# Optimization experiments

Measured on AMD Instinct MI355X. Metric: run time of the kernel, lower is better.

The kernel has to match this reference:

```python
import jax, jax.numpy as jnp
import numpy as np
from jax import lax

EPS = 1e-5


def _conv(x, w, b, stride, pad):
    # x: [B,C,H,W], w: [O,I,kh,kw] (NCHW / OIHW, same as torch Conv2d)
    y = lax.conv_general_dilated(
        x, w, window_strides=stride,
        padding=[(pad[0], pad[0]), (pad[1], pad[1])],
        dimension_numbers=('NCHW', 'OIHW', 'NCHW'))
    return y + b[None, :, None, None]


def _bn(x, gamma, beta, mean, var):
    # BatchNorm2d in eval mode (running statistics)
    inv = gamma / jnp.sqrt(var + EPS)
    return x * inv[None, :, None, None] + (beta - mean * inv)[None, :, None, None]


def _mask_time(x, lens):
    # Vectorized replacement of the per-sample narrow/fill loop:
    # zero every time step >= lens[b] along the last axis.
    t = jnp.arange(x.shape[3])
    keep = (t[None, :] < lens[:, None]).astype(x.dtype)  # [B, W]
    return x * keep[:, None, None, :]


def _new_len(lens, kernel_w, stride_w, pad_w):
    # matches get_new_sequence_lengths for Conv2d with dilation 1
    return (lens + 2 * pad_w - (kernel_w - 1) - 1) // stride_w + 1


def _forward(inputs, seq_lengths,
             w1, b1, g1, be1, m1, v1,
             w2, b2, g2, be2, m2, v2):
    lens = seq_lengths.astype(jnp.int32)
    # layer 1: Conv2d(1,32,(41,11),(2,2),(20,5))
    x = _conv(inputs, w1, b1, (2, 2), (20, 5))
    lens = _new_len(lens, 11, 2, 5)
    x = _mask_time(x, lens)
    # BatchNorm2d(32) -> mask
    x = _mask_time(_bn(x, g1, be1, m1, v1), lens)
    # Hardtanh(0,20) -> mask
    x = _mask_time(jnp.clip(x, 0.0, 20.0), lens)
    # layer 2: Conv2d(32,32,(21,11),(2,1),(10,5))
    x = _conv(x, w2, b2, (2, 1), (10, 5))
    lens = _new_len(lens, 11, 1, 5)
    x = _mask_time(x, lens)
    x = _mask_time(_bn(x, g2, be2, m2, v2), lens)
    x = _mask_time(jnp.clip(x, 0.0, 20.0), lens)
    return x, lens


def setup_inputs() -> dict:
    key = jax.random.key(0)
    ks = jax.random.split(key, 8)
    inputs = jax.random.normal(ks[0], (32, 1, 161, 1024), dtype=jnp.float32)
    seq_lengths = jax.random.randint(ks[1], (32,), 1, 1024, dtype=jnp.int32)
    w1 = jax.random.normal(ks[2], (32, 1, 41, 11), dtype=jnp.float32) * 0.05
    b1 = jax.random.normal(ks[3], (32,), dtype=jnp.float32) * 0.05
    w2 = jax.random.normal(ks[4], (32, 32, 21, 11), dtype=jnp.float32) * 0.02
    b2 = jax.random.normal(ks[5], (32,), dtype=jnp.float32) * 0.05
    g1 = jnp.ones((32,), jnp.float32)
    be1 = jnp.zeros((32,), jnp.float32)
    m1 = jax.random.normal(ks[6], (32,), dtype=jnp.float32) * 0.1
    v1 = jnp.ones((32,), jnp.float32)
    g2 = jnp.ones((32,), jnp.float32)
    be2 = jnp.zeros((32,), jnp.float32)
    m2 = jax.random.normal(ks[7], (32,), dtype=jnp.float32) * 0.1
    v2 = jnp.ones((32,), jnp.float32)
    return {"inputs": inputs, "seq_lengths": seq_lengths,
            "w1": w1, "b1": b1, "g1": g1, "be1": be1, "m1": m1, "v1": v1,
            "w2": w2, "b2": b2, "g2": g2, "be2": be2, "m2": m2, "v2": v2}


def reference(inputs, seq_lengths, w1, b1, g1, be1, m1, v1,
              w2, b2, g2, be2, m2, v2):
    return _forward(inputs, seq_lengths, w1, b1, g1, be1, m1, v1,
                    w2, b2, g2, be2, m2, v2)
```

## Files before the change

### kernel.cpp

```cpp
#include <hip/hip_runtime.h>
#include <math.h>

#define B_    32
#define H_IN  161
#define W_IN  1024
#define C1_   32
#define H1_   81
#define W1_   512
#define C2_   32
#define H2_   41
#define W2_   512

#define OUT_X_SZ ((size_t)B_ * C2_ * H2_ * W2_)

#define WF2_B    0u
#define WF1_B    563200u
#define SCSH_B   609280u
#define LENS1_B  609792u
#define XG_B     609920u

#define WF2_N    281600
#define WF1_N    23040

typedef __bf16 v8bf __attribute__((ext_vector_type(8)));
typedef float v16f __attribute__((ext_vector_type(16)));

static __device__ __forceinline__ unsigned short f2bf(float f) {
    unsigned int u = __float_as_uint(f);
    unsigned int r = (u + 0x7fffu + ((u >> 16) & 1u)) >> 16;
    return (unsigned short)r;
}

__global__ void prep_kernel(const float* __restrict__ w1, const float* __restrict__ b1,
                            const float* __restrict__ g1, const float* __restrict__ be1,
                            const float* __restrict__ m1, const float* __restrict__ v1,
                            const float* __restrict__ w2, const float* __restrict__ b2,
                            const float* __restrict__ g2, const float* __restrict__ be2,
                            const float* __restrict__ m2, const float* __restrict__ v2,
                            const int* __restrict__ lens,
                            unsigned short* __restrict__ wf1, unsigned short* __restrict__ wf2,
                            float* __restrict__ scsh, int* __restrict__ lens1,
                            float* __restrict__ out_lens)
{
    const int i = blockIdx.x * blockDim.x + threadIdx.x;
    const int stride = gridDim.x * blockDim.x;

    for (int idx = i; idx < WF2_N; idx += stride) {
        int j  = idx & 7;
        int l  = (idx >> 3) & 63;
        int f  = idx >> 9;
        int ch = f & 1;
        int kwkh = f >> 1;
        int kw  = kwkh % 11;
        int khp = kwkh / 11;
        int kh  = khp - 2;
        int oc = l & 31;
        int c  = ch * 16 + ((l >> 5) << 3) + j;
        wf2[idx] = (kh >= 0 && kh < 21)
                 ? f2bf(w2[((oc * 32 + c) * 21 + kh) * 11 + kw]) : (unsigned short)0;
    }
    for (int idx = i; idx < WF1_N; idx += stride) {
        int j   = idx & 7;
        int l   = (idx >> 3) & 63;
        int khp = idx >> 9;
        int kh  = khp - 2;
        int k   = ((l >> 5) << 3) + j;
        int oc  = l & 31;
        wf1[idx] = (k < 11 && kh >= 0 && kh < 41)
                 ? f2bf(w1[oc * 451 + kh * 11 + k]) : (unsigned short)0;
    }
    if (i < 32) {
        float s1 = g1[i] / sqrtf(v1[i] + 1e-5f);
        scsh[i]      = s1;
        scsh[32 + i] = b1[i] * s1 + be1[i] - m1[i] * s1;
        float s2 = g2[i] / sqrtf(v2[i] + 1e-5f);
        scsh[64 + i] = s2;
        scsh[96 + i] = b2[i] * s2 + be2[i] - m2[i] * s2;
        int l1 = (lens[i] - 1) / 2 + 1;
        if (l1 > W1_) l1 = W1_;
        lens1[i] = l1;
        out_lens[i] = (float)l1;
    }
}

__global__ __launch_bounds__(256) void conv1_mfma(
    const float* __restrict__ x,
    const unsigned short* __restrict__ wf1,
    const float* __restrict__ scsh,
    const int* __restrict__ lens1,
    unsigned short* __restrict__ xg)
{
    const int t    = threadIdx.x;
    const int lane = t & 63;
    const int l31  = lane & 31;
    const int lhi  = lane >> 5;
    const int wv   = t >> 6;
    const int w0   = blockIdx.x * 256;
    const int hp   = blockIdx.y;
    const int b    = blockIdx.z;
    const int h0   = hp * 2;
    const bool h1ok = (h0 + 1) < H1_;

    __shared__ unsigned int srow[2][264];

    v16f acc[2][2];
#pragma unroll
    for (int hh = 0; hh < 2; ++hh)
#pragma unroll
        for (int nt = 0; nt < 2; ++nt)
#pragma unroll
            for (int q = 0; q < 16; ++q) acc[hh][nt][q] = 0.f;

    const int r0 = 2 * h0 - 20;
    const int cb = 2 * w0 - 5;
    const float* xb = x + (size_t)b * (H_IN * W_IN);

    const int dwbase = wv * 64 + l31 + 4 * lhi;

    {
        float a0 = 0.f, a1 = 0.f, c0v = 0.f, c1v = 0.f;
        if (r0 >= 0 && r0 < H_IN) {
            const float* src = xb + (size_t)r0 * W_IN;
            int c0 = cb + 2 * t;
            if ((unsigned)c0 < (unsigned)W_IN)       a0 = src[c0];
            if ((unsigned)(c0 + 1) < (unsigned)W_IN) a1 = src[c0 + 1];
            if (t < 7) {
                int c1 = cb + 2 * (256 + t);
                if ((unsigned)c1 < (unsigned)W_IN)       c0v = src[c1];
                if ((unsigned)(c1 + 1) < (unsigned)W_IN) c1v = src[c1 + 1];
            }
        }
        srow[0][t] = (unsigned int)f2bf(a0) | ((unsigned int)f2bf(a1) << 16);
        if (t < 7)
            srow[0][256 + t] = (unsigned int)f2bf(c0v) | ((unsigned int)f2bf(c1v) << 16);
    }
    __syncthreads();

    const uint4* wf1q = (const uint4*)wf1;

    for (int kp = 0; kp < 43; ++kp) {
        const int p = kp & 1;
        const int rn = r0 + kp + 1;
        const bool rv = (kp < 42) && (rn >= 0) && (rn < H_IN);

        float a0 = 0.f, a1 = 0.f, c0v = 0.f, c1v = 0.f;
        if (rv) {
            const float* src = xb + (size_t)rn * W_IN;
            int c0 = cb + 2 * t;
            if ((unsigned)c0 < (unsigned)W_IN)       a0 = src[c0];
            if ((unsigned)(c0 + 1) < (unsigned)W_IN) a1 = src[c0 + 1];
            if (t < 7) {
                int c1 = cb + 2 * (256 + t);
                if ((unsigned)c1 < (unsigned)W_IN)       c0v = src[c1];
                if ((unsigned)(c1 + 1) < (unsigned)W_IN) c1v = src[c1 + 1];
            }
        }

        const int r = r0 + kp;
        if (r >= 0 && r < H_IN) {
            uint4 a0u = wf1q[(kp + 2) * 32 + lane];
            uint4 a1u = wf1q[kp * 32 + lane];
            v8bf A0 = __builtin_bit_cast(v8bf, a0u);
            v8bf A1 = __builtin_bit_cast(v8bf, a1u);
            const unsigned int* bp = &srow[p][0];
            uint4 bu0, bu1;
            {
                int dw = dwbase;
                bu0.x = bp[dw]; bu0.y = bp[dw + 1]; bu0.z = bp[dw + 2]; bu0.w = bp[dw + 3];
                dw += 32;
                bu1.x = bp[dw]; bu1.y = bp[dw + 1]; bu1.z = bp[dw + 2]; bu1.w = bp[dw + 3];
            }
            v8bf B0 = __builtin_bit_cast(v8bf, bu0);
            v8bf B1 = __builtin_bit_cast(v8bf, bu1);
            acc[0][0] = __builtin_amdgcn_mfma_f32_32x32x16_bf16(A0, B0, acc[0][0], 0, 0, 0);
            acc[0][1] = __builtin_amdgcn_mfma_f32_32x32x16_bf16(A0, B1, acc[0][1], 0, 0, 0);
            acc[1][0] = __builtin_amdgcn_mfma_f32_32x32x16_bf16(A1, B0, acc[1][0], 0, 0, 0);
            acc[1][1] = __builtin_amdgcn_mfma_f32_32x32x16_bf16(A1, B1, acc[1][1], 0, 0, 0);
        }

        if (rv) {
            srow[p ^ 1][t] = (unsigned int)f2bf(a0) | ((unsigned int)f2bf(a1) << 16);
            if (t < 7)
                srow[p ^ 1][256 + t] = (unsigned int)f2bf(c0v) | ((unsigned int)f2bf(c1v) << 16);
        }
        __syncthreads();
    }

    const int l1 = lens1[b];
#pragma unroll
    for (int hh = 0; hh < 2; ++hh) {
        if (hh == 1 && !h1ok) break;
        const int h = h0 + hh;
#pragma unroll
        for (int nt = 0; nt < 2; ++nt) {
            const int w = w0 + wv * 64 + nt * 32 + l31;
            const bool keep = (w < l1);
            unsigned short* dp = xg + (((size_t)b * H1_ + h) * W1_ + w) * 32;
#pragma unroll
            for (int rq = 0; rq < 4; ++rq) {
                unsigned int wd[2];
#pragma unroll
                for (int d = 0; d < 2; ++d) {
                    int rg = rq * 4 + d * 2;
                    int oc = 8 * rq + 4 * lhi + d * 2;
                    float av0 = acc[hh][nt][rg];
                    float av1 = acc[hh][nt][rg + 1];
                    float v0 = fminf(fmaxf(fmaf(av0, scsh[oc],     scsh[32 + oc]), 0.f), 20.f);
                    float v1 = fminf(fmaxf(fmaf(av1, scsh[oc + 1], scsh[33 + oc]), 0.f), 20.f);
                    if (!keep) { v0 = 0.f; v1 = 0.f; }
                    wd[d] = (unsigned int)f2bf(v0) | ((unsigned int)f2bf(v1) << 16);
                }
                uint2 u; u.x = wd[0]; u.y = wd[1];
                *(uint2*)(dp + 8 * rq + 4 * lhi) = u;
            }
        }
    }
}

#define ROWB 21280

__global__ __launch_bounds__(256, 3) void conv2_mfma(
    const unsigned short* __restrict__ xg,
    const unsigned short* __restrict__ wf2,
    const float* __restrict__ scsh,
    const int* __restrict__ lens1,
    float* __restrict__ out)
{
    const int t    = threadIdx.x;
    const int lane = t & 63;
    const int l31  = lane & 31;
    const int lhi  = lane >> 5;
    const int wv   = t >> 6;

    const int id   = blockIdx.x;
    const int sid  = (id & 7) * 168 + (id >> 3);
    const int wblk = sid & 1;
    const int bh   = sid >> 1;
    const int hp   = bh % 21;
    const int b    = bh / 21;
    const int h0   = hp * 2;
    const bool h1ok = (h0 + 1) < H2_;
    const int w0B  = wblk << 8;

    __shared__ __align__(16) char sbuf[2 * ROWB];

    v16f acc[2][2];
#pragma unroll
    for (int hh = 0; hh < 2; ++hh)
#pragma unroll
        for (int nt = 0; nt < 2; ++nt)
#pragma unroll
            for (int q = 0; q < 16; ++q) acc[hh][nt][q] = 0.f;

    const int st_lds = (t >> 2) * 80 + (t & 3) * 16;
    const int rd_lds = (wv * 64 + l31) * 80 + lhi * 16;

    const unsigned short* xb = xg + (size_t)b * (H1_ * W1_ * 32);
    const int r0 = 2 * h0 - 10;

    {
        int r = r0;
        if (r >= 0 && r < H1_) {
            const unsigned short* xrow = xb + (size_t)r * (W1_ * 32);
#pragma unroll
            for (int it = 0; it < 5; ++it) {
                int i = t + it * 256;
                int wp = (i >> 2) + w0B - 5;
                uint4 z; z.x = z.y = z.z = z.w = 0u;
                if (i < 1064 && wp >= 0 && wp < W1_)
                    z = *(const uint4*)(xrow + (size_t)wp * 32 + (i & 3) * 8);
                if (i < 1064)
                    *(uint4*)(sbuf + st_lds + it * 5120) = z;
            }
        }
    }
    __syncthreads();

    const uint4* wq = (const uint4*)wf2;

    for (int kp = 0; kp < 23; ++kp) {
        const int p = kp & 1;
        const int rn = r0 + kp + 1;
        const bool stage_next = (kp < 22) && (rn >= 0) && (rn < H1_);

        uint4 g0, g1, g2, g3, g4;
        g0.x=g0.y=g0.z=g0.w=0u; g1=g0; g2=g0; g3=g0; g4=g0;
        if (stage_next) {
            const unsigned short* xrow = xb + (size_t)rn * (W1_ * 32);
            const int wbase = (t >> 2) + w0B - 5;
            const int ck = (t & 3) * 8;
            if (wbase >= 0 && wbase < W1_)                 g0 = *(const uint4*)(xrow + (size_t)wbase * 32 + ck);
            if (wbase + 64 >= 0 && wbase + 64 < W1_)       g1 = *(const uint4*)(xrow + (size_t)(wbase + 64) * 32 + ck);
            if (wbase + 128 < W1_)                         g2 = *(const uint4*)(xrow + (size_t)(wbase + 128) * 32 + ck);
            if (wbase + 192 < W1_)                         g3 = *(const uint4*)(xrow + (size_t)(wbase + 192) * 32 + ck);
            if (t < 40 && wbase + 256 < W1_)               g4 = *(const uint4*)(xrow + (size_t)(wbase + 256) * 32 + ck);
        }

        const int r = r0 + kp;
        if (r >= 0 && r < H1_) {
            const int f0 = (kp + 2) * 22;
            const int f1 = kp * 22;
            const char* bbase = sbuf + p * ROWB + rd_lds;
            __builtin_amdgcn_s_setprio(1);
#pragma unroll
            for (int kw = 0; kw < 11; ++kw) {
#pragma unroll
                for (int ch = 0; ch < 2; ++ch) {
                    uint4 a0u = wq[(f0 + kw * 2 + ch) * 64 + lane];
                    uint4 a1u = wq[(f1 + kw * 2 + ch) * 64 + lane];
                    uint4 b0u = *(const uint4*)(bbase + kw * 80 + ch * 32);
                    uint4 b1u = *(const uint4*)(bbase + 2560 + kw * 80 + ch * 32);
                    v8bf A0 = __builtin_bit_cast(v8bf, a0u);
                    v8bf A1 = __builtin_bit_cast(v8bf, a1u);
                    v8bf B0 = __builtin_bit_cast(v8bf, b0u);
                    v8bf B1 = __builtin_bit_cast(v8bf, b1u);
                    acc[0][0] = __builtin_amdgcn_mfma_f32_32x32x16_bf16(A0, B0, acc[0][0], 0, 0, 0);
                    acc[0][1] = __builtin_amdgcn_mfma_f32_32x32x16_bf16(A0, B1, acc[0][1], 0, 0, 0);
                    acc[1][0] = __builtin_amdgcn_mfma_f32_32x32x16_bf16(A1, B0, acc[1][0], 0, 0, 0);
                    acc[1][1] = __builtin_amdgcn_mfma_f32_32x32x16_bf16(A1, B1, acc[1][1], 0, 0, 0);
                }
            }
            __builtin_amdgcn_s_setprio(0);
        }

        if (stage_next) {
            char* wb = sbuf + (p ^ 1) * ROWB + st_lds;
            *(uint4*)(wb)            = g0;
            *(uint4*)(wb + 5120)     = g1;
            *(uint4*)(wb + 2 * 5120) = g2;
            *(uint4*)(wb + 3 * 5120) = g3;
            if (t < 40) *(uint4*)(wb + 4 * 5120) = g4;
        }
        __syncthreads();
    }

    const int l2 = lens1[b];
#pragma unroll
    for (int hh = 0; hh < 2; ++hh) {
        if (hh == 1 && !h1ok) break;
        const int h = h0 + hh;
#pragma unroll
        for (int nt = 0; nt < 2; ++nt) {
            const int w = w0B + wv * 64 + nt * 32 + l31;
            const bool keep = (w < l2);
#pragma unroll
            for (int reg = 0; reg < 16; ++reg) {
                const int oc = (reg & 3) + 8 * (reg >> 2) + 4 * lhi;
                float v = fmaf(acc[hh][nt][reg], scsh[64 + oc], scsh[96 + oc]);
                v = fminf(fmaxf(v, 0.f), 20.f);
                out[(((size_t)b * C2_ + oc) * H2_ + h) * W2_ + w] = keep ? v : 0.f;
            }
        }
    }
}

extern "C" void kernel_launch(void* const* d_in, const int* in_sizes, int n_in,
                              void* d_out, int out_size, void* d_ws, size_t ws_size,
                              hipStream_t stream) {
    const float* inputs = (const float*)d_in[0];
    const int*   slen   = (const int*)d_in[1];
    const float* w1 = (const float*)d_in[2];
    const float* b1 = (const float*)d_in[3];
    const float* g1 = (const float*)d_in[4];
    const float* be1 = (const float*)d_in[5];
    const float* m1 = (const float*)d_in[6];
    const float* v1 = (const float*)d_in[7];
    const float* w2 = (const float*)d_in[8];
    const float* b2 = (const float*)d_in[9];
    const float* g2 = (const float*)d_in[10];
    const float* be2 = (const float*)d_in[11];
    const float* m2 = (const float*)d_in[12];
    const float* v2 = (const float*)d_in[13];

    char* ws = (char*)d_ws;
    unsigned short* wf2  = (unsigned short*)(ws + WF2_B);
    unsigned short* wf1  = (unsigned short*)(ws + WF1_B);
    float*          scsh = (float*)(ws + SCSH_B);
    int*            lens1 = (int*)(ws + LENS1_B);
    unsigned short* xg   = (unsigned short*)(ws + XG_B);

    float* out_x    = (float*)d_out;
    float* out_lens = out_x + OUT_X_SZ;

    hipLaunchKernelGGL(prep_kernel, dim3(256), dim3(256), 0, stream,
                       w1, b1, g1, be1, m1, v1, w2, b2, g2, be2, m2, v2,
                       slen, wf1, wf2, scsh, lens1, out_lens);

    hipLaunchKernelGGL(conv1_mfma, dim3(2, 41, B_), dim3(256), 0, stream,
                       inputs, wf1, scsh, lens1, xg);

    hipLaunchKernelGGL(conv2_mfma, dim3(1344), dim3(256), 0, stream,
                       xg, wf2, scsh, lens1, out_x);
}
```

Measured before the change: 533.9 us.

## Stage a 55-row input slab in LDS and compute four output row pairs per block

conv1 now loads a slab of 55 input rows into shared memory once per block and computes four output row-pairs from it. Before, each block streamed 43 rows with a double-buffered row and a barrier per row. This cuts redundant global reads of overlapping input rows (about 4x reuse) and removes the per-row synchronisation. In exchange it uses about 58 KB of LDS per block, which limits occupancy (launch bounds ask for 2 blocks), and cuts the grid from 41 to 11 row segments, leaving fewer blocks to hide latency.

```diff
diff --git a/kernel.cpp b/kernel.cpp
--- a/kernel.cpp
+++ b/kernel.cpp
@@ -83,7 +83,10 @@
     }
 }
 
-__global__ __launch_bounds__(256) void conv1_mfma(
+#define S1ROWS 55
+#define S1U    264
+
+__global__ __launch_bounds__(256, 2) void conv1_mfma(
     const float* __restrict__ x,
     const unsigned short* __restrict__ wf1,
     const float* __restrict__ scsh,
@@ -96,73 +99,68 @@
     const int lhi  = lane >> 5;
     const int wv   = t >> 6;
     const int w0   = blockIdx.x * 256;
-    const int hp   = blockIdx.y;
+    const int seg  = blockIdx.y;
     const int b    = blockIdx.z;
-    const int h0   = hp * 2;
-    const bool h1ok = (h0 + 1) < H1_;
-
-    __shared__ unsigned int srow[2][264];
-
-    v16f acc[2][2];
-#pragma unroll
-    for (int hh = 0; hh < 2; ++hh)
-#pragma unroll
-        for (int nt = 0; nt < 2; ++nt)
-#pragma unroll
-            for (int q = 0; q < 16; ++q) acc[hh][nt][q] = 0.f;
-
-    const int r0 = 2 * h0 - 20;
-    const int cb = 2 * w0 - 5;
+
+    __shared__ unsigned int slab[S1ROWS * S1U];
+
+    const int rbase = 16 * seg - 20;
+    const int cb    = 2 * w0 - 5;
     const float* xb = x + (size_t)b * (H_IN * W_IN);
 
-    const int dwbase = wv * 64 + l31 + 4 * lhi;
-
-    {
-        float a0 = 0.f, a1 = 0.f, c0v = 0.f, c1v = 0.f;
-        if (r0 >= 0 && r0 < H_IN) {
-            const float* src = xb + (size_t)r0 * W_IN;
-            int c0 = cb + 2 * t;
-            if ((unsigned)c0 < (unsigned)W_IN)       a0 = src[c0];
-            if ((unsigned)(c0 + 1) < (unsigned)W_IN) a1 = src[c0 + 1];
-            if (t < 7) {
-                int c1 = cb + 2 * (256 + t);
-                if ((unsigned)c1 < (unsigned)W_IN)       c0v = src[c1];
-                if ((unsigned)(c1 + 1) < (unsigned)W_IN) c1v = src[c1 + 1];
-            }
-        }
-        srow[0][t] = (unsigned int)f2bf(a0) | ((unsigned int)f2bf(a1) << 16);
-        if (t < 7)
-            srow[0][256 + t] = (unsigned int)f2bf(c0v) | ((unsigned int)f2bf(c1v) << 16);
+    for (int rho = wv; rho < S1ROWS; rho += 4) {
+        const int r = rbase + rho;
+        const bool rowok = (r >= 0) && (r < H_IN);
+        const float* src = xb + (size_t)r * W_IN;
+        unsigned int* drow = &slab[rho * S1U];
+#pragma unroll
+        for (int j = 0; j < 4; ++j) {
+            const int cp = lane + 64 * j;
+            const int c  = cb + 2 * cp;
+            float a0 = 0.f, a1 = 0.f;
+            if (rowok) {
+                if ((unsigned)c < (unsigned)W_IN)       a0 = src[c];
+                if ((unsigned)(c + 1) < (unsigned)W_IN) a1 = src[c + 1];
+            }
+            drow[cp] = (unsigned int)f2bf(a0) | ((unsigned int)f2bf(a1) << 16);
+        }
+        if (lane < 8) {
+            const int cp = lane + 256;
+            const int c  = cb + 2 * cp;
+            float a0 = 0.f, a1 = 0.f;
+            if (rowok) {
+                if ((unsigned)c < (unsigned)W_IN)       a0 = src[c];
+                if ((unsigned)(c + 1) < (unsigned)W_IN) a1 = src[c + 1];
+            }
+            drow[cp] = (unsigned int)f2bf(a0) | ((unsigned int)f2bf(a1) << 16);
+        }
     }
     __syncthreads();
 
     const uint4* wf1q = (const uint4*)wf1;
-
-    for (int kp = 0; kp < 43; ++kp) {
-        const int p = kp & 1;
-        const int rn = r0 + kp + 1;
-        const bool rv = (kp < 42) && (rn >= 0) && (rn < H_IN);
-
-        float a0 = 0.f, a1 = 0.f, c0v = 0.f, c1v = 0.f;
-        if (rv) {
-            const float* src = xb + (size_t)rn * W_IN;
-            int c0 = cb + 2 * t;
-            if ((unsigned)c0 < (unsigned)W_IN)       a0 = src[c0];
-            if ((unsigned)(c0 + 1) < (unsigned)W_IN) a1 = src[c0 + 1];
-            if (t < 7) {
-                int c1 = cb + 2 * (256 + t);
-                if ((unsigned)c1 < (unsigned)W_IN)       c0v = src[c1];
-                if ((unsigned)(c1 + 1) < (unsigned)W_IN) c1v = src[c1 + 1];
-            }
-        }
-
-        const int r = r0 + kp;
-        if (r >= 0 && r < H_IN) {
+    const int dwbase  = wv * 64 + l31 + 4 * lhi;
+    const int l1      = lens1[b];
+
+    for (int q = 0; q < 4; ++q) {
+        const int pr = seg * 4 + q;
+        if (pr > 40) break;
+        const int h0 = pr * 2;
+        const bool h1ok = (h0 + 1) < H1_;
+
+        v16f acc[2][2];
+#pragma unroll
+        for (int hh = 0; hh < 2; ++hh)
+#pragma unroll
+            for (int nt = 0; nt < 2; ++nt)
+#pragma unroll
+                for (int qq = 0; qq < 16; ++qq) acc[hh][nt][qq] = 0.f;
+
+        const unsigned int* base = &slab[(4 * q) * S1U];
+
+        for (int kp = 0; kp < 43; ++kp) {
             uint4 a0u = wf1q[(kp + 2) * 32 + lane];
             uint4 a1u = wf1q[kp * 32 + lane];
-            v8bf A0 = __builtin_bit_cast(v8bf, a0u);
-            v8bf A1 = __builtin_bit_cast(v8bf, a1u);
-            const unsigned int* bp = &srow[p][0];
+            const unsigned int* bp = base + kp * S1U;
             uint4 bu0, bu1;
             {
                 int dw = dwbase;
@@ -170,6 +168,8 @@
                 dw += 32;
                 bu1.x = bp[dw]; bu1.y = bp[dw + 1]; bu1.z = bp[dw + 2]; bu1.w = bp[dw + 3];
             }
+            v8bf A0 = __builtin_bit_cast(v8bf, a0u);
+            v8bf A1 = __builtin_bit_cast(v8bf, a1u);
             v8bf B0 = __builtin_bit_cast(v8bf, bu0);
             v8bf B1 = __builtin_bit_cast(v8bf, bu1);
             acc[0][0] = __builtin_amdgcn_mfma_f32_32x32x16_bf16(A0, B0, acc[0][0], 0, 0, 0);
@@ -178,40 +178,32 @@
             acc[1][1] = __builtin_amdgcn_mfma_f32_32x32x16_bf16(A1, B1, acc[1][1], 0, 0, 0);
         }
 
-        if (rv) {
-            srow[p ^ 1][t] = (unsigned int)f2bf(a0) | ((unsigned int)f2bf(a1) << 16);
-            if (t < 7)
-                srow[p ^ 1][256 + t] = (unsigned int)f2bf(c0v) | ((unsigned int)f2bf(c1v) << 16);
-        }
-        __syncthreads();
-    }
-
-    const int l1 = lens1[b];
-#pragma unroll
-    for (int hh = 0; hh < 2; ++hh) {
-        if (hh == 1 && !h1ok) break;
-        const int h = h0 + hh;
-#pragma unroll
-        for (int nt = 0; nt < 2; ++nt) {
-            const int w = w0 + wv * 64 + nt * 32 + l31;
-            const bool keep = (w < l1);
-            unsigned short* dp = xg + (((size_t)b * H1_ + h) * W1_ + w) * 32;
-#pragma unroll
-            for (int rq = 0; rq < 4; ++rq) {
-                unsigned int wd[2];
-#pragma unroll
-                for (int d = 0; d < 2; ++d) {
-                    int rg = rq * 4 + d * 2;
-                    int oc = 8 * rq + 4 * lhi + d * 2;
-                    float av0 = acc[hh][nt][rg];
-                    float av1 = acc[hh][nt][rg + 1];
-                    float v0 = fminf(fmaxf(fmaf(av0, scsh[oc],     scsh[32 + oc]), 0.f), 20.f);
-                    float v1 = fminf(fmaxf(fmaf(av1, scsh[oc + 1], scsh[33 + oc]), 0.f), 20.f);
-                    if (!keep) { v0 = 0.f; v1 = 0.f; }
-                    wd[d] = (unsigned int)f2bf(v0) | ((unsigned int)f2bf(v1) << 16);
+#pragma unroll
+        for (int hh = 0; hh < 2; ++hh) {
+            if (hh == 1 && !h1ok) break;
+            const int h = h0 + hh;
+#pragma unroll
+            for (int nt = 0; nt < 2; ++nt) {
+                const int w = w0 + wv * 64 + nt * 32 + l31;
+                const bool keep = (w < l1);
+                unsigned short* dp = xg + (((size_t)b * H1_ + h) * W1_ + w) * 32;
+#pragma unroll
+                for (int rq = 0; rq < 4; ++rq) {
+                    unsigned int wd[2];
+#pragma unroll
+                    for (int d = 0; d < 2; ++d) {
+                        int rg = rq * 4 + d * 2;
+                        int oc = 8 * rq + 4 * lhi + d * 2;
+                        float av0 = acc[hh][nt][rg];
+                        float av1 = acc[hh][nt][rg + 1];
+                        float v0 = fminf(fmaxf(fmaf(av0, scsh[oc],     scsh[32 + oc]), 0.f), 20.f);
+                        float v1 = fminf(fmaxf(fmaf(av1, scsh[oc + 1], scsh[33 + oc]), 0.f), 20.f);
+                        if (!keep) { v0 = 0.f; v1 = 0.f; }
+                        wd[d] = (unsigned int)f2bf(v0) | ((unsigned int)f2bf(v1) << 16);
+                    }
+                    uint2 u; u.x = wd[0]; u.y = wd[1];
+                    *(uint2*)(dp + 8 * rq + 4 * lhi) = u;
                 }
-                uint2 u; u.x = wd[0]; u.y = wd[1];
-                *(uint2*)(dp + 8 * rq + 4 * lhi) = u;
             }
         }
     }
@@ -386,7 +378,7 @@
                        w1, b1, g1, be1, m1, v1, w2, b2, g2, be2, m2, v2,
                        slen, wf1, wf2, scsh, lens1, out_lens);
 
-    hipLaunchKernelGGL(conv1_mfma, dim3(2, 41, B_), dim3(256), 0, stream,
+    hipLaunchKernelGGL(conv1_mfma, dim3(2, 11, B_), dim3(256), 0, stream,
                        inputs, wf1, scsh, lens1, xg);
 
     hipLaunchKernelGGL(conv2_mfma, dim3(1344), dim3(256), 0, stream,
```

New measurement: 544.1 us. About the same (+1.9%).

## Widen conv2 tile to full output row per block with padded LDS stride

Applied to the files above, without the earlier changes.

Each conv2 block now covers all 512 output columns instead of 256, so each wave computes 4 N-tiles per weight fragment. This halves the grid and the redundant halo loads and weight fetches per output. The LDS row stride changes from 80 to 72 bytes to alter bank mapping. It doubles the accumulator registers, so launch bounds drop to 2 blocks per SM, and the 672-block grid may leave the CUs less evenly loaded.

```diff
diff --git a/kernel.cpp b/kernel.cpp
--- a/kernel.cpp
+++ b/kernel.cpp
@@ -217,9 +217,11 @@
     }
 }
 
-#define ROWB 21280
-
-__global__ __launch_bounds__(256, 3) void conv2_mfma(
+#define C2POSN  522
+#define C2STR   72
+#define C2BUFB  (C2POSN * C2STR)
+
+__global__ __launch_bounds__(256, 2) void conv2_mfma(
     const unsigned short* __restrict__ xg,
     const unsigned short* __restrict__ wf2,
     const float* __restrict__ scsh,
@@ -232,75 +234,79 @@
     const int lhi  = lane >> 5;
     const int wv   = t >> 6;
 
-    const int id   = blockIdx.x;
-    const int sid  = (id & 7) * 168 + (id >> 3);
-    const int wblk = sid & 1;
-    const int bh   = sid >> 1;
-    const int hp   = bh % 21;
-    const int b    = bh / 21;
-    const int h0   = hp * 2;
+    const int id  = blockIdx.x;
+    const int sid = (id & 7) * 84 + (id >> 3);
+    const int hp  = sid % 21;
+    const int b   = sid / 21;
+    const int h0  = hp * 2;
     const bool h1ok = (h0 + 1) < H2_;
-    const int w0B  = wblk << 8;
-
-    __shared__ __align__(16) char sbuf[2 * ROWB];
-
-    v16f acc[2][2];
+
+    __shared__ __align__(16) char sbuf[2 * C2BUFB];
+
+    v16f acc[2][4];
 #pragma unroll
     for (int hh = 0; hh < 2; ++hh)
 #pragma unroll
-        for (int nt = 0; nt < 2; ++nt)
+        for (int nt = 0; nt < 4; ++nt)
 #pragma unroll
             for (int q = 0; q < 16; ++q) acc[hh][nt][q] = 0.f;
-
-    const int st_lds = (t >> 2) * 80 + (t & 3) * 16;
-    const int rd_lds = (wv * 64 + l31) * 80 + lhi * 16;
 
     const unsigned short* xb = xg + (size_t)b * (H1_ * W1_ * 32);
     const int r0 = 2 * h0 - 10;
+
+    int soff[9], ldso[9];
+    bool vld[9];
+#pragma unroll
+    for (int i = 0; i < 9; ++i) {
+        int c   = t + 256 * i;
+        int pos = c >> 2;
+        int sg  = c & 3;
+        int wcol = pos - 5;
+        vld[i]  = (c < 2088) && (wcol >= 0) && (wcol < W1_);
+        soff[i] = wcol * 64 + sg * 16;
+        ldso[i] = pos * C2STR + sg * 16;
+    }
 
     {
         int r = r0;
         if (r >= 0 && r < H1_) {
-            const unsigned short* xrow = xb + (size_t)r * (W1_ * 32);
-#pragma unroll
-            for (int it = 0; it < 5; ++it) {
-                int i = t + it * 256;
-                int wp = (i >> 2) + w0B - 5;
-                uint4 z; z.x = z.y = z.z = z.w = 0u;
-                if (i < 1064 && wp >= 0 && wp < W1_)
-                    z = *(const uint4*)(xrow + (size_t)wp * 32 + (i & 3) * 8);
-                if (i < 1064)
-                    *(uint4*)(sbuf + st_lds + it * 5120) = z;
+            const char* xrow = (const char*)(xb + (size_t)r * (W1_ * 32));
+#pragma unroll
+            for (int i = 0; i < 9; ++i) {
+                if (t + 256 * i < 2088) {
+                    uint4 z; z.x = z.y = z.z = z.w = 0u;
+                    if (vld[i]) z = *(const uint4*)(xrow + soff[i]);
+                    *(uint4*)(sbuf + ldso[i]) = z;
+                }
             }
         }
     }
     __syncthreads();
 
     const uint4* wq = (const uint4*)wf2;
+    const int rdbase = (wv * 128 + l31) * C2STR + lhi * 16;
+
+    uint4 g[9];
 
     for (int kp = 0; kp < 23; ++kp) {
         const int p = kp & 1;
         const int rn = r0 + kp + 1;
         const bool stage_next = (kp < 22) && (rn >= 0) && (rn < H1_);
 
-        uint4 g0, g1, g2, g3, g4;
-        g0.x=g0.y=g0.z=g0.w=0u; g1=g0; g2=g0; g3=g0; g4=g0;
         if (stage_next) {
-            const unsigned short* xrow = xb + (size_t)rn * (W1_ * 32);
-            const int wbase = (t >> 2) + w0B - 5;
-            const int ck = (t & 3) * 8;
-            if (wbase >= 0 && wbase < W1_)                 g0 = *(const uint4*)(xrow + (size_t)wbase * 32 + ck);
-            if (wbase + 64 >= 0 && wbase + 64 < W1_)       g1 = *(const uint4*)(xrow + (size_t)(wbase + 64) * 32 + ck);
-            if (wbase + 128 < W1_)                         g2 = *(const uint4*)(xrow + (size_t)(wbase + 128) * 32 + ck);
-            if (wbase + 192 < W1_)                         g3 = *(const uint4*)(xrow + (size_t)(wbase + 192) * 32 + ck);
-            if (t < 40 && wbase + 256 < W1_)               g4 = *(const uint4*)(xrow + (size_t)(wbase + 256) * 32 + ck);
+            const char* xrow = (const char*)(xb + (size_t)rn * (W1_ * 32));
+#pragma unroll
+            for (int i = 0; i < 9; ++i) {
+                g[i].x = g[i].y = g[i].z = g[i].w = 0u;
+                if (vld[i]) g[i] = *(const uint4*)(xrow + soff[i]);
+            }
         }
 
         const int r = r0 + kp;
         if (r >= 0 && r < H1_) {
             const int f0 = (kp + 2) * 22;
             const int f1 = kp * 22;
-            const char* bbase = sbuf + p * ROWB + rd_lds;
+            const char* bbase = sbuf + p * C2BUFB + rdbase;
             __builtin_amdgcn_s_setprio(1);
 #pragma unroll
             for (int kw = 0; kw < 11; ++kw) {
@@ -308,28 +314,34 @@
                 for (int ch = 0; ch < 2; ++ch) {
                     uint4 a0u = wq[(f0 + kw * 2 + ch) * 64 + lane];
                     uint4 a1u = wq[(f1 + kw * 2 + ch) * 64 + lane];
-                    uint4 b0u = *(const uint4*)(bbase + kw * 80 + ch * 32);
-                    uint4 b1u = *(const uint4*)(bbase + 2560 + kw * 80 + ch * 32);
                     v8bf A0 = __builtin_bit_cast(v8bf, a0u);
                     v8bf A1 = __builtin_bit_cast(v8bf, a1u);
+                    uint4 b0u = *(const uint4*)(bbase + kw * C2STR + ch * 32);
+                    uint4 b1u = *(const uint4*)(bbase + (32 * C2STR) + kw * C2STR + ch * 32);
+                    uint4 b2u = *(const uint4*)(bbase + (64 * C2STR) + kw * C2STR + ch * 32);
+                    uint4 b3u = *(const uint4*)(bbase + (96 * C2STR) + kw * C2STR + ch * 32);
                     v8bf B0 = __builtin_bit_cast(v8bf, b0u);
                     v8bf B1 = __builtin_bit_cast(v8bf, b1u);
+                    v8bf B2 = __builtin_bit_cast(v8bf, b2u);
+                    v8bf B3 = __builtin_bit_cast(v8bf, b3u);
                     acc[0][0] = __builtin_amdgcn_mfma_f32_32x32x16_bf16(A0, B0, acc[0][0], 0, 0, 0);
                     acc[0][1] = __builtin_amdgcn_mfma_f32_32x32x16_bf16(A0, B1, acc[0][1], 0, 0, 0);
+                    acc[0][2] = __builtin_amdgcn_mfma_f32_32x32x16_bf16(A0, B2, acc[0][2], 0, 0, 0);
+                    acc[0][3] = __builtin_amdgcn_mfma_f32_32x32x16_bf16(A0, B3, acc[0][3], 0, 0, 0);
                     acc[1][0] = __builtin_amdgcn_mfma_f32_32x32x16_bf16(A1, B0, acc[1][0], 0, 0, 0);
                     acc[1][1] = __builtin_amdgcn_mfma_f32_32x32x16_bf16(A1, B1, acc[1][1], 0, 0, 0);
+                    acc[1][2] = __builtin_amdgcn_mfma_f32_32x32x16_bf16(A1, B2, acc[1][2], 0, 0, 0);
+                    acc[1][3] = __builtin_amdgcn_mfma_f32_32x32x16_bf16(A1, B3, acc[1][3], 0, 0, 0);
                 }
             }
             __builtin_amdgcn_s_setprio(0);
         }
 
         if (stage_next) {
-            char* wb = sbuf + (p ^ 1) * ROWB + st_lds;
-            *(uint4*)(wb)            = g0;
-            *(uint4*)(wb + 5120)     = g1;
-            *(uint4*)(wb + 2 * 5120) = g2;
-            *(uint4*)(wb + 3 * 5120) = g3;
-            if (t < 40) *(uint4*)(wb + 4 * 5120) = g4;
+            char* db = sbuf + (p ^ 1) * C2BUFB;
+#pragma unroll
+            for (int i = 0; i < 8; ++i) *(uint4*)(db + ldso[i]) = g[i];
+            if (t < 40) *(uint4*)(db + ldso[8]) = g[8];
         }
         __syncthreads();
     }
@@ -340,8 +352,8 @@
         if (hh == 1 && !h1ok) break;
         const int h = h0 + hh;
 #pragma unroll
-        for (int nt = 0; nt < 2; ++nt) {
-            const int w = w0B + wv * 64 + nt * 32 + l31;
+        for (int nt = 0; nt < 4; ++nt) {
+            const int w = wv * 128 + nt * 32 + l31;
             const bool keep = (w < l2);
 #pragma unroll
             for (int reg = 0; reg < 16; ++reg) {
@@ -389,6 +401,6 @@
     hipLaunchKernelGGL(conv1_mfma, dim3(2, 41, B_), dim3(256), 0, stream,
                        inputs, wf1, scsh, lens1, xg);
 
-    hipLaunchKernelGGL(conv2_mfma, dim3(1344), dim3(256), 0, stream,
+    hipLaunchKernelGGL(conv2_mfma, dim3(672), dim3(256), 0, stream,
                        xg, wf2, scsh, lens1, out_x);
 }
```

Measured after the change: 1.105 ms. 107% more time.
